# Optimization experiments

Measured on AMD Instinct MI355X. Metric: run time of the kernel, lower is better.

The kernel has to match this reference:

```python
import jax, jax.numpy as jnp
import numpy as np

N_NODES = 100000
N_EDGES = 1600000
IN_DIM = 128
OUT_DIM = 64


def setup_inputs() -> dict:
    key = jax.random.key(0)
    k1, k2, k3, k4, k5 = jax.random.split(key, 5)
    x = jax.random.normal(k1, (N_NODES, IN_DIM), dtype=jnp.float32)
    edge_index = jax.random.randint(k2, (2, N_EDGES), 0, N_NODES, dtype=jnp.int64)
    # xavier_uniform for Linear(in,out): bound = sqrt(6/(in+out))
    wb = float(np.sqrt(6.0 / (IN_DIM + OUT_DIM)))
    W = jax.random.uniform(k3, (OUT_DIM, IN_DIM), dtype=jnp.float32, minval=-wb, maxval=wb)
    # xavier_uniform on a.unsqueeze(0): fan_in=out_dim, fan_out=1
    ab = float(np.sqrt(6.0 / (OUT_DIM + 1)))
    a_src = jax.random.uniform(k4, (OUT_DIM,), dtype=jnp.float32, minval=-ab, maxval=b if (b := ab) else ab)
    a_dst = jax.random.uniform(k5, (OUT_DIM,), dtype=jnp.float32, minval=-ab, maxval=ab)
    return {"x": x, "edge_index": edge_index, "W": W, "a_src": a_src, "a_dst": a_dst}


def reference(x, edge_index, W, a_src, a_dst):
    # h = x @ W^T : [N, out_dim]
    h = x @ W.T
    src, dst = edge_index[0], edge_index[1]
    # per-node attention logits, gathered per edge (cheaper than gathering h twice for the dot)
    s_src = h @ a_src  # [N]
    s_dst = h @ a_dst  # [N]
    e = s_src[src] + s_dst[dst]  # [E]
    e = jnp.where(e >= 0, e, 0.2 * e)  # LeakyReLU(0.2)
    e = jnp.clip(e, -10.0, 10.0)
    alpha_num = jnp.exp(e)
    denom = jax.ops.segment_sum(alpha_num, dst, num_segments=N_NODES)  # [N]
    alpha = alpha_num / (denom[dst] + 1e-9)  # [E]; dropout is identity (eval / p=0)
    msgs = alpha[:, None] * h[src]  # [E, out_dim]
    out = jax.ops.segment_sum(msgs, dst, num_segments=N_NODES)  # [N, out_dim]
    return out
```

## Files before the change

### kernel.cpp

```cpp
#include <hip/hip_runtime.h>
#include <math.h>

#define NN 100000
#define NE 1600000
#define BKB 7
#define BSZ 128
#define NBKT 782
#define LPS  (NBKT + 1)
#define EPB 2048
#define NPB ((NE + EPB - 1) / EPB)
#define TOTC (NBKT * NPB)
#define SBLK 2048
#define NSB ((TOTC + SBLK - 1) / SBLK)
#define LBUF2 2560
#define EVC 5

typedef unsigned int uint;
typedef unsigned short ushort;
typedef __attribute__((ext_vector_type(8))) short bfx8;
typedef __attribute__((ext_vector_type(4))) float f32x4;

static __device__ __forceinline__ ushort f2bf(float f) {
  uint u = __float_as_uint(f);
  uint r = (u + 0x7fffu + ((u >> 16) & 1u)) >> 16;
  return (ushort)r;
}
static __device__ __forceinline__ float bf2f(ushort v) {
  return __uint_as_float((uint)v << 16);
}
static __device__ __forceinline__ bfx8 cvt8(float4 a, float4 b) {
  bfx8 r;
  r[0] = (short)f2bf(a.x); r[1] = (short)f2bf(a.y);
  r[2] = (short)f2bf(a.z); r[3] = (short)f2bf(a.w);
  r[4] = (short)f2bf(b.x); r[5] = (short)f2bf(b.y);
  r[6] = (short)f2bf(b.z); r[7] = (short)f2bf(b.w);
  return r;
}

__global__ __launch_bounds__(256) void k_h(
    const float* __restrict__ x, const float* __restrict__ W,
    const float* __restrict__ a_src, const float* __restrict__ a_dst,
    ushort* __restrict__ h16, float* __restrict__ ssrc, float* __restrict__ sdst)
{
  __shared__ __align__(16) ushort ws[64 * 128];
  const int t = threadIdx.x;
  const int base = blockIdx.x * 64;
  const float4* x4 = (const float4*)x;
  const float4* W4 = (const float4*)W;

#pragma unroll
  for (int q = 0; q < 8; ++q) {
    int f = q * 256 + t;
    int row = f >> 5, c4 = f & 31;
    float4 v = W4[f];
    ushort4 pk = make_ushort4(f2bf(v.x), f2bf(v.y), f2bf(v.z), f2bf(v.w));
    int byte = row * 256 + ((c4 * 8) ^ ((row & 7) << 4));
    *(ushort4*)((char*)ws + byte) = pk;
  }

  const int wid = t >> 6;
  const int lane = t & 63;
  const int lg = lane >> 4;
  const int lr = lane & 15;

  const int node = base + wid * 16 + lr;
  const bool ok = node < NN;
  const float4* xr = x4 + (size_t)node * 32;

  float4 xa[4][2];
#pragma unroll
  for (int ks = 0; ks < 4; ++ks) {
    xa[ks][0] = ok ? xr[ks * 8 + lg * 2]     : make_float4(0.f, 0.f, 0.f, 0.f);
    xa[ks][1] = ok ? xr[ks * 8 + lg * 2 + 1] : make_float4(0.f, 0.f, 0.f, 0.f);
  }
  __syncthreads();

  f32x4 acc[4];
#pragma unroll
  for (int ng = 0; ng < 4; ++ng) acc[ng] = (f32x4){0.f, 0.f, 0.f, 0.f};

#pragma unroll
  for (int ks = 0; ks < 4; ++ks) {
    int kb = ks * 64 + lg * 16;
    bfx8 af = cvt8(xa[ks][0], xa[ks][1]);
    bfx8 bfr[4];
#pragma unroll
    for (int ng = 0; ng < 4; ++ng) {
      int row = ng * 16 + lr;
      bfr[ng] = *(const bfx8*)((const char*)ws + row * 256 + (kb ^ ((row & 7) << 4)));
    }
#pragma unroll
    for (int ng = 0; ng < 4; ++ng)
      acc[ng] = __builtin_amdgcn_mfma_f32_16x16x32_bf16(af, bfr[ng], acc[ng], 0, 0, 0);
  }

  float as_[4], ad_[4];
#pragma unroll
  for (int ng = 0; ng < 4; ++ng) { as_[ng] = a_src[ng * 16 + lr]; ad_[ng] = a_dst[ng * 16 + lr]; }
#pragma unroll
  for (int r = 0; r < 4; ++r) {
    int nout = base + wid * 16 + lg * 4 + r;
    float ps = 0.f, pd = 0.f;
#pragma unroll
    for (int ng = 0; ng < 4; ++ng) { ps += acc[ng][r] * as_[ng]; pd += acc[ng][r] * ad_[ng]; }
#pragma unroll
    for (int m = 1; m < 16; m <<= 1) { ps += __shfl_xor(ps, m); pd += __shfl_xor(pd, m); }
    if (lr == 0 && nout < NN) { ssrc[nout] = ps; sdst[nout] = pd; }
    if (nout < NN) {
#pragma unroll
      for (int ng = 0; ng < 4; ++ng)
        h16[(size_t)nout * 64 + ng * 16 + lr] = f2bf(acc[ng][r]);
    }
  }
}

__global__ __launch_bounds__(512) void k_sort(const int* __restrict__ ei,
                                              int* __restrict__ cnt_cm,
                                              int* __restrict__ lpre,
                                              int* __restrict__ stage)
{
  __shared__ int hh[NBKT];
  __shared__ int sums[512];
  __shared__ int sbuf[EPB];
  const int t = threadIdx.x, c = blockIdx.x;
  for (int i = t; i < NBKT; i += 512) hh[i] = 0;
  __syncthreads();

  const int base = c * EPB;
  const int nloc = min(EPB, NE - base);
  int my_src[EPB / 512], my_dst[EPB / 512];
#pragma unroll
  for (int q = 0; q < EPB / 512; ++q) {
    int e = base + q * 512 + t;
    if (e < NE) {
      my_src[q] = ei[e];
      my_dst[q] = ei[NE + e];
      atomicAdd(&hh[my_dst[q] >> BKB], 1);
    } else my_dst[q] = -1;
  }
  __syncthreads();

  int i0 = 2 * t, i1 = 2 * t + 1;
  int v0 = (i0 < NBKT) ? hh[i0] : 0;
  int v1 = (i1 < NBKT) ? hh[i1] : 0;
  sums[t] = v0 + v1;
  __syncthreads();
  for (int off = 1; off < 512; off <<= 1) {
    int u = (t >= off) ? sums[t - off] : 0;
    __syncthreads();
    sums[t] += u;
    __syncthreads();
  }
  int ex0 = sums[t] - (v0 + v1);
  if (i0 < NBKT) {
    hh[i0] = ex0;
    lpre[c * LPS + i0] = ex0;
    cnt_cm[(size_t)c * NBKT + i0] = v0;
  }
  if (i1 < NBKT) {
    hh[i1] = ex0 + v0;
    lpre[c * LPS + i1] = ex0 + v0;
    cnt_cm[(size_t)c * NBKT + i1] = v1;
  }
  if (t == 0) lpre[c * LPS + NBKT] = nloc;
  __syncthreads();

#pragma unroll
  for (int q = 0; q < EPB / 512; ++q) {
    if (my_dst[q] >= 0) {
      int dst = my_dst[q], src = my_src[q];
      int pos = atomicAdd(&hh[dst >> BKB], 1);
      sbuf[pos] = src | ((dst & (BSZ - 1)) << 24);
    }
  }
  __syncthreads();
#pragma unroll
  for (int q = 0; q < EPB / 512; ++q) {
    int i = q * 512 + t;
    if (i < nloc) stage[base + i] = sbuf[i];
  }
}

__global__ __launch_bounds__(256) void k_tr(const int* __restrict__ cnt_cm,
                                            const int* __restrict__ lpre,
                                            int* __restrict__ cnt,
                                            int* __restrict__ lpreT)
{
  __shared__ int tileA[32][33];
  __shared__ int tileB[32][33];
  int cb = blockIdx.x * 32, bb = blockIdx.y * 32;
  int tx = threadIdx.x & 31, ty = threadIdx.x >> 5;
  for (int r = ty; r < 32; r += 8) {
    int c = cb + r, b = bb + tx;
    bool in = (c < NPB && b < NBKT);
    tileA[r][tx] = in ? cnt_cm[(size_t)c * NBKT + b] : 0;
    tileB[r][tx] = in ? lpre[(size_t)c * LPS + b] : 0;
  }
  __syncthreads();
  for (int r = ty; r < 32; r += 8) {
    int b = bb + r, c = cb + tx;
    if (b < NBKT && c < NPB) {
      cnt[(size_t)b * NPB + c] = tileA[tx][r];
      lpreT[(size_t)b * NPB + c] = tileB[tx][r];
    }
  }
}

__global__ __launch_bounds__(256) void k_scanA(const int* __restrict__ cnt,
                                               int* __restrict__ partials)
{
  __shared__ int sm[256];
  int t = threadIdx.x, b = blockIdx.x;
  const int4* c4 = (const int4*)(cnt + b * SBLK + t * 8);
  int4 u = c4[0], v = c4[1];
  sm[t] = u.x + u.y + u.z + u.w + v.x + v.y + v.z + v.w;
  __syncthreads();
  for (int s = 128; s > 0; s >>= 1) { if (t < s) sm[t] += sm[t + s]; __syncthreads(); }
  if (t == 0) partials[b] = sm[0];
}

__global__ __launch_bounds__(512) void k_scanB(int* __restrict__ partials,
                                               int* __restrict__ boff)
{
  __shared__ int sm[512];
  int t = threadIdx.x;
  int v = (t < NSB) ? partials[t] : 0;
  sm[t] = v;
  __syncthreads();
  for (int off = 1; off < 512; off <<= 1) {
    int u = (t >= off) ? sm[t - off] : 0;
    __syncthreads();
    sm[t] += u;
    __syncthreads();
  }
  if (t < NSB) partials[t] = sm[t] - v;
  if (t == 0) boff[NBKT] = NE;
}

__global__ __launch_bounds__(256) void k_scanC(int* __restrict__ cnt,
                                               const int* __restrict__ partials,
                                               int* __restrict__ boff)
{
  __shared__ int sm[256];
  int t = threadIdx.x, b = blockIdx.x;
  int base = b * SBLK + t * 8;
  int4* c4 = (int4*)(cnt + base);
  int4 u = c4[0], v = c4[1];
  int tot = u.x + u.y + u.z + u.w + v.x + v.y + v.z + v.w;
  sm[t] = tot;
  __syncthreads();
  for (int off = 1; off < 256; off <<= 1) {
    int w = (t >= off) ? sm[t - off] : 0;
    __syncthreads();
    sm[t] += w;
    __syncthreads();
  }
  int run = partials[b] + sm[t] - tot;
  int e[8] = {u.x, u.y, u.z, u.w, v.x, v.y, v.z, v.w};
  int ex[8];
#pragma unroll
  for (int k = 0; k < 8; ++k) { ex[k] = run; run += e[k]; }
#pragma unroll
  for (int k = 0; k < 8; ++k) {
    int idx = base + k;
    if (idx < TOTC && idx % NPB == 0) boff[idx / NPB] = ex[k];
  }
  c4[0] = make_int4(ex[0], ex[1], ex[2], ex[3]);
  c4[1] = make_int4(ex[4], ex[5], ex[6], ex[7]);
}

__global__ __launch_bounds__(512) void k_fuse(const int* __restrict__ boff,
                                              const int* __restrict__ pcnt,
                                              const int* __restrict__ lpreT,
                                              const int* __restrict__ stage,
                                              const float* __restrict__ ssrc,
                                              const float* __restrict__ sdst,
                                              const ushort* __restrict__ h16,
                                              float* __restrict__ out)
{
  __shared__ int2 lbuf[LBUF2];
  __shared__ int pcl[NPB + 1];
  __shared__ int lpb[NPB];
  __shared__ int nh[BSZ];
  __shared__ int nst[BSZ];
  __shared__ int cur[BSZ];
  __shared__ float sdl[BSZ];
  const int b = blockIdx.x, t = threadIdx.x;
  const int e_beg = boff[b], e_end = boff[b + 1];
  const int m = e_end - e_beg;

  for (int j = t; j < NPB; j += 512) {
    pcl[j] = pcnt[(size_t)b * NPB + j] - e_beg;
    lpb[j] = lpreT[(size_t)b * NPB + j];
  }
  if (t == 0) pcl[NPB] = m;
  if (t < BSZ) {
    nh[t] = 0;
    int node = (b << BKB) + t;
    sdl[t] = (node < NN) ? sdst[node] : 0.f;
  }
  __syncthreads();

  int ev[EVC];
  float ssv[EVC];
  int ne = 0;
#pragma unroll
  for (int q = 0; q < EVC; ++q) {
    int i = q * 512 + t;
    if (i < m) {
      int lo = 0, hi = NPB;
      while (hi - lo > 1) { int mid = (lo + hi) >> 1; if (pcl[mid] <= i) lo = mid; else hi = mid; }
      ev[q] = stage[(size_t)lo * EPB + lpb[lo] + (i - pcl[lo])];
      ssv[q] = ssrc[ev[q] & 0xFFFFFF];
      atomicAdd(&nh[((uint)ev[q]) >> 24], 1);
      ne = q + 1;
    }
  }
  __syncthreads();

  int v0 = (t < BSZ) ? nh[t] : 0;
  if (t < BSZ) nst[t] = v0;
  __syncthreads();
  for (int off = 1; off < BSZ; off <<= 1) {
    int u = (t >= off && t < BSZ) ? nst[t - off] : 0;
    __syncthreads();
    if (t < BSZ) nst[t] += u;
    __syncthreads();
  }
  if (t < BSZ) { int ex = nst[t] - v0; cur[t] = ex; nh[t] = ex; }
  __syncthreads();

  int slots[EVC];
  float alph[EVC];
#pragma unroll
  for (int q = 0; q < EVC; ++q) {
    if (q < ne) {
      int dl = ((uint)ev[q]) >> 24;
      slots[q] = atomicAdd(&cur[dl], 1);
      float e = ssv[q] + sdl[dl];
      e = (e >= 0.f) ? e : 0.2f * e;
      e = fminf(fmaxf(e, -10.f), 10.f);
      alph[q] = __expf(e);
    }
  }
#pragma unroll
  for (int q = 0; q < EVC; ++q)
    if (q < ne) lbuf[slots[q]] = make_int2(ev[q] & 0xFFFFFF, __float_as_int(alph[q]));
  __syncthreads();

  const int sid = t >> 4;
  const int l16 = t & 15;
  const int half = l16 >> 3, l8 = l16 & 7;
  const uint4* h4 = (const uint4*)h16;
#pragma unroll
  for (int r = 0; r < 4; ++r) {
    int nl = sid + 32 * r;
    int beg = nh[nl];
    int end = nst[nl];
    float a0 = 0.f, a1 = 0.f, a2 = 0.f, a3 = 0.f;
    float a4 = 0.f, a5 = 0.f, a6 = 0.f, a7 = 0.f;
    float den = 0.f;
    int last = end - 1;
    for (int j = beg; j < end; j += 8) {
#pragma unroll
      for (int p = 0; p < 4; ++p) {
        int idx = j + p * 2 + half;
        int2 e = lbuf[min(idx, last)];
        float a = (idx < end) ? __int_as_float(e.y) : 0.f;
        uint4 hq = h4[(size_t)e.x * 8 + l8];
        den += a;
        a0 += a * bf2f((ushort)(hq.x & 0xffff));
        a1 += a * bf2f((ushort)(hq.x >> 16));
        a2 += a * bf2f((ushort)(hq.y & 0xffff));
        a3 += a * bf2f((ushort)(hq.y >> 16));
        a4 += a * bf2f((ushort)(hq.z & 0xffff));
        a5 += a * bf2f((ushort)(hq.z >> 16));
        a6 += a * bf2f((ushort)(hq.w & 0xffff));
        a7 += a * bf2f((ushort)(hq.w >> 16));
      }
    }
    a0 += __shfl_xor(a0, 8);
    a1 += __shfl_xor(a1, 8);
    a2 += __shfl_xor(a2, 8);
    a3 += __shfl_xor(a3, 8);
    a4 += __shfl_xor(a4, 8);
    a5 += __shfl_xor(a5, 8);
    a6 += __shfl_xor(a6, 8);
    a7 += __shfl_xor(a7, 8);
    den += __shfl_xor(den, 8);
    int node = (b << BKB) + nl;
    if (node < NN) {
      float inv = 1.f / (den + 1e-9f);
      float4 o = half ? make_float4(a4 * inv, a5 * inv, a6 * inv, a7 * inv)
                      : make_float4(a0 * inv, a1 * inv, a2 * inv, a3 * inv);
      ((float4*)out)[(size_t)node * 16 + l8 * 2 + half] = o;
    }
  }
}

extern "C" void kernel_launch(void* const* d_in, const int* in_sizes, int n_in,
                              void* d_out, int out_size, void* d_ws, size_t ws_size,
                              hipStream_t stream)
{
  const float* x     = (const float*)d_in[0];
  const int*   ei    = (const int*)d_in[1];
  const float* W     = (const float*)d_in[2];
  const float* a_src = (const float*)d_in[3];
  const float* a_dst = (const float*)d_in[4];
  float* out = (float*)d_out;

  char* p = (char*)d_ws;
  auto alloc = [&](size_t bytes) -> char* {
    char* r = p;
    p += (bytes + 255) & ~(size_t)255;
    return r;
  };
  ushort* h16    = (ushort*)alloc((size_t)NN * 64 * 2);
  float* ssrc    = (float*)alloc((size_t)NN * 4);
  float* sdst    = (float*)alloc((size_t)NN * 4);
  int*   cnt     = (int*)alloc((size_t)NSB * SBLK * 4);
  int*   cnt_cm  = (int*)alloc((size_t)NPB * NBKT * 4);
  int*   lpre    = (int*)alloc((size_t)NPB * LPS * 4);
  int*   lpreT   = (int*)alloc((size_t)NBKT * NPB * 4);
  int*   boff    = (int*)alloc((size_t)(NBKT + 1) * 4);
  int*   partials= (int*)alloc((size_t)NSB * 4);
  int*   stage   = (int*)alloc((size_t)NPB * EPB * 4);

  k_h<<<(NN + 63) / 64, 256, 0, stream>>>(x, W, a_src, a_dst, h16, ssrc, sdst);
  k_sort<<<NPB, 512, 0, stream>>>(ei, cnt_cm, lpre, stage);
  k_tr<<<dim3((NPB + 31) / 32, (NBKT + 31) / 32), 256, 0, stream>>>(cnt_cm, lpre, cnt, lpreT);
  k_scanA<<<NSB, 256, 0, stream>>>(cnt, partials);
  k_scanB<<<1, 512, 0, stream>>>(partials, boff);
  k_scanC<<<NSB, 256, 0, stream>>>(cnt, partials, boff);
  k_fuse<<<NBKT, 512, 0, stream>>>(boff, cnt, lpreT, stage, ssrc, sdst, h16, out);
}
```

Baseline: 86.29 us.

## Merge projection and edge bucket-sort kernels into one interleaved launch

Combines the node projection GEMM kernel and the per-chunk edge bucket sort into a single launch. Even blocks compute 128 nodes of h, s_src and s_dst with 512 threads, and odd blocks perform the counting-sort of one edge chunk, sharing a 16KB shared-memory buffer. This removes one kernel launch boundary and lets the compute-bound MFMA work overlap with the memory- and atomic-bound sort work. The cost is a larger block size for the GEMM path and shared memory sized for the larger of the two roles, which may reduce occupancy. Block count HB+NPB (782+782) matches the even/odd interleave because HB equals NPB.

```diff
diff --git a/kernel.cpp b/kernel.cpp
--- a/kernel.cpp
+++ b/kernel.cpp
@@ -9,6 +9,7 @@
 #define LPS  (NBKT + 1)
 #define EPB 2048
 #define NPB ((NE + EPB - 1) / EPB)
+#define HB  782
 #define TOTC (NBKT * NPB)
 #define SBLK 2048
 #define NSB ((TOTC + SBLK - 1) / SBLK)
@@ -37,147 +38,149 @@
   return r;
 }
 
-__global__ __launch_bounds__(256) void k_h(
+__global__ __launch_bounds__(512) void k_hs(
     const float* __restrict__ x, const float* __restrict__ W,
     const float* __restrict__ a_src, const float* __restrict__ a_dst,
-    ushort* __restrict__ h16, float* __restrict__ ssrc, float* __restrict__ sdst)
-{
-  __shared__ __align__(16) ushort ws[64 * 128];
+    const int* __restrict__ ei,
+    ushort* __restrict__ h16, float* __restrict__ ssrc, float* __restrict__ sdst,
+    int* __restrict__ cnt_cm, int* __restrict__ lpre, int* __restrict__ stage)
+{
+  __shared__ __align__(16) char smem[16384];
   const int t = threadIdx.x;
-  const int base = blockIdx.x * 64;
-  const float4* x4 = (const float4*)x;
-  const float4* W4 = (const float4*)W;
-
-#pragma unroll
-  for (int q = 0; q < 8; ++q) {
-    int f = q * 256 + t;
-    int row = f >> 5, c4 = f & 31;
-    float4 v = W4[f];
-    ushort4 pk = make_ushort4(f2bf(v.x), f2bf(v.y), f2bf(v.z), f2bf(v.w));
-    int byte = row * 256 + ((c4 * 8) ^ ((row & 7) << 4));
-    *(ushort4*)((char*)ws + byte) = pk;
-  }
-
-  const int wid = t >> 6;
-  const int lane = t & 63;
-  const int lg = lane >> 4;
-  const int lr = lane & 15;
-
-  const int node = base + wid * 16 + lr;
-  const bool ok = node < NN;
-  const float4* xr = x4 + (size_t)node * 32;
-
-  float4 xa[4][2];
-#pragma unroll
-  for (int ks = 0; ks < 4; ++ks) {
-    xa[ks][0] = ok ? xr[ks * 8 + lg * 2]     : make_float4(0.f, 0.f, 0.f, 0.f);
-    xa[ks][1] = ok ? xr[ks * 8 + lg * 2 + 1] : make_float4(0.f, 0.f, 0.f, 0.f);
-  }
-  __syncthreads();
-
-  f32x4 acc[4];
-#pragma unroll
-  for (int ng = 0; ng < 4; ++ng) acc[ng] = (f32x4){0.f, 0.f, 0.f, 0.f};
-
-#pragma unroll
-  for (int ks = 0; ks < 4; ++ks) {
-    int kb = ks * 64 + lg * 16;
-    bfx8 af = cvt8(xa[ks][0], xa[ks][1]);
-    bfx8 bfr[4];
-#pragma unroll
-    for (int ng = 0; ng < 4; ++ng) {
-      int row = ng * 16 + lr;
-      bfr[ng] = *(const bfx8*)((const char*)ws + row * 256 + (kb ^ ((row & 7) << 4)));
-    }
-#pragma unroll
-    for (int ng = 0; ng < 4; ++ng)
-      acc[ng] = __builtin_amdgcn_mfma_f32_16x16x32_bf16(af, bfr[ng], acc[ng], 0, 0, 0);
-  }
-
-  float as_[4], ad_[4];
-#pragma unroll
-  for (int ng = 0; ng < 4; ++ng) { as_[ng] = a_src[ng * 16 + lr]; ad_[ng] = a_dst[ng * 16 + lr]; }
-#pragma unroll
-  for (int r = 0; r < 4; ++r) {
-    int nout = base + wid * 16 + lg * 4 + r;
-    float ps = 0.f, pd = 0.f;
-#pragma unroll
-    for (int ng = 0; ng < 4; ++ng) { ps += acc[ng][r] * as_[ng]; pd += acc[ng][r] * ad_[ng]; }
-#pragma unroll
-    for (int m = 1; m < 16; m <<= 1) { ps += __shfl_xor(ps, m); pd += __shfl_xor(pd, m); }
-    if (lr == 0 && nout < NN) { ssrc[nout] = ps; sdst[nout] = pd; }
-    if (nout < NN) {
+
+  if ((blockIdx.x & 1) == 0) {
+    ushort* ws = (ushort*)smem;
+    const int hb = blockIdx.x >> 1;
+    const int base = hb * 128;
+    const float4* x4 = (const float4*)x;
+    const float4* W4 = (const float4*)W;
+
+#pragma unroll
+    for (int q = 0; q < 4; ++q) {
+      int f = q * 512 + t;
+      int row = f >> 5, c4 = f & 31;
+      float4 v = W4[f];
+      ushort4 pk = make_ushort4(f2bf(v.x), f2bf(v.y), f2bf(v.z), f2bf(v.w));
+      int byte = row * 256 + ((c4 * 8) ^ ((row & 7) << 4));
+      *(ushort4*)((char*)ws + byte) = pk;
+    }
+
+    const int wid = t >> 6;
+    const int lane = t & 63;
+    const int lg = lane >> 4;
+    const int lr = lane & 15;
+
+    const int node = base + wid * 16 + lr;
+    const bool ok = node < NN;
+    const float4* xr = x4 + (size_t)node * 32;
+
+    float4 xa[4][2];
+#pragma unroll
+    for (int ks = 0; ks < 4; ++ks) {
+      xa[ks][0] = ok ? xr[ks * 8 + lg * 2]     : make_float4(0.f, 0.f, 0.f, 0.f);
+      xa[ks][1] = ok ? xr[ks * 8 + lg * 2 + 1] : make_float4(0.f, 0.f, 0.f, 0.f);
+    }
+    __syncthreads();
+
+    f32x4 acc[4];
+#pragma unroll
+    for (int ng = 0; ng < 4; ++ng) acc[ng] = (f32x4){0.f, 0.f, 0.f, 0.f};
+
+#pragma unroll
+    for (int ks = 0; ks < 4; ++ks) {
+      int kb = ks * 64 + lg * 16;
+      bfx8 af = cvt8(xa[ks][0], xa[ks][1]);
+      bfx8 bfr[4];
+#pragma unroll
+      for (int ng = 0; ng < 4; ++ng) {
+        int row = ng * 16 + lr;
+        bfr[ng] = *(const bfx8*)((const char*)ws + row * 256 + (kb ^ ((row & 7) << 4)));
+      }
 #pragma unroll
       for (int ng = 0; ng < 4; ++ng)
-        h16[(size_t)nout * 64 + ng * 16 + lr] = f2bf(acc[ng][r]);
-    }
-  }
-}
-
-__global__ __launch_bounds__(512) void k_sort(const int* __restrict__ ei,
-                                              int* __restrict__ cnt_cm,
-                                              int* __restrict__ lpre,
-                                              int* __restrict__ stage)
-{
-  __shared__ int hh[NBKT];
-  __shared__ int sums[512];
-  __shared__ int sbuf[EPB];
-  const int t = threadIdx.x, c = blockIdx.x;
-  for (int i = t; i < NBKT; i += 512) hh[i] = 0;
-  __syncthreads();
-
-  const int base = c * EPB;
-  const int nloc = min(EPB, NE - base);
-  int my_src[EPB / 512], my_dst[EPB / 512];
-#pragma unroll
-  for (int q = 0; q < EPB / 512; ++q) {
-    int e = base + q * 512 + t;
-    if (e < NE) {
-      my_src[q] = ei[e];
-      my_dst[q] = ei[NE + e];
-      atomicAdd(&hh[my_dst[q] >> BKB], 1);
-    } else my_dst[q] = -1;
-  }
-  __syncthreads();
-
-  int i0 = 2 * t, i1 = 2 * t + 1;
-  int v0 = (i0 < NBKT) ? hh[i0] : 0;
-  int v1 = (i1 < NBKT) ? hh[i1] : 0;
-  sums[t] = v0 + v1;
-  __syncthreads();
-  for (int off = 1; off < 512; off <<= 1) {
-    int u = (t >= off) ? sums[t - off] : 0;
-    __syncthreads();
-    sums[t] += u;
-    __syncthreads();
-  }
-  int ex0 = sums[t] - (v0 + v1);
-  if (i0 < NBKT) {
-    hh[i0] = ex0;
-    lpre[c * LPS + i0] = ex0;
-    cnt_cm[(size_t)c * NBKT + i0] = v0;
-  }
-  if (i1 < NBKT) {
-    hh[i1] = ex0 + v0;
-    lpre[c * LPS + i1] = ex0 + v0;
-    cnt_cm[(size_t)c * NBKT + i1] = v1;
-  }
-  if (t == 0) lpre[c * LPS + NBKT] = nloc;
-  __syncthreads();
-
-#pragma unroll
-  for (int q = 0; q < EPB / 512; ++q) {
-    if (my_dst[q] >= 0) {
-      int dst = my_dst[q], src = my_src[q];
-      int pos = atomicAdd(&hh[dst >> BKB], 1);
-      sbuf[pos] = src | ((dst & (BSZ - 1)) << 24);
-    }
-  }
-  __syncthreads();
-#pragma unroll
-  for (int q = 0; q < EPB / 512; ++q) {
-    int i = q * 512 + t;
-    if (i < nloc) stage[base + i] = sbuf[i];
+        acc[ng] = __builtin_amdgcn_mfma_f32_16x16x32_bf16(af, bfr[ng], acc[ng], 0, 0, 0);
+    }
+
+    float as_[4], ad_[4];
+#pragma unroll
+    for (int ng = 0; ng < 4; ++ng) { as_[ng] = a_src[ng * 16 + lr]; ad_[ng] = a_dst[ng * 16 + lr]; }
+#pragma unroll
+    for (int r = 0; r < 4; ++r) {
+      int nout = base + wid * 16 + lg * 4 + r;
+      float ps = 0.f, pd = 0.f;
+#pragma unroll
+      for (int ng = 0; ng < 4; ++ng) { ps += acc[ng][r] * as_[ng]; pd += acc[ng][r] * ad_[ng]; }
+#pragma unroll
+      for (int m = 1; m < 16; m <<= 1) { ps += __shfl_xor(ps, m); pd += __shfl_xor(pd, m); }
+      if (lr == 0 && nout < NN) { ssrc[nout] = ps; sdst[nout] = pd; }
+      if (nout < NN) {
+#pragma unroll
+        for (int ng = 0; ng < 4; ++ng)
+          h16[(size_t)nout * 64 + ng * 16 + lr] = f2bf(acc[ng][r]);
+      }
+    }
+  } else {
+    int* hh   = (int*)smem;
+    int* sums = (int*)(smem + 3200);
+    int* sbuf = (int*)(smem + 5248);
+    const int c = blockIdx.x >> 1;
+
+    for (int i = t; i < NBKT; i += 512) hh[i] = 0;
+    __syncthreads();
+
+    const int base = c * EPB;
+    const int nloc = min(EPB, NE - base);
+    int my_src[EPB / 512], my_dst[EPB / 512];
+#pragma unroll
+    for (int q = 0; q < EPB / 512; ++q) {
+      int e = base + q * 512 + t;
+      if (e < NE) {
+        my_src[q] = ei[e];
+        my_dst[q] = ei[NE + e];
+        atomicAdd(&hh[my_dst[q] >> BKB], 1);
+      } else my_dst[q] = -1;
+    }
+    __syncthreads();
+
+    int i0 = 2 * t, i1 = 2 * t + 1;
+    int v0 = (i0 < NBKT) ? hh[i0] : 0;
+    int v1 = (i1 < NBKT) ? hh[i1] : 0;
+    sums[t] = v0 + v1;
+    __syncthreads();
+    for (int off = 1; off < 512; off <<= 1) {
+      int u = (t >= off) ? sums[t - off] : 0;
+      __syncthreads();
+      sums[t] += u;
+      __syncthreads();
+    }
+    int ex0 = sums[t] - (v0 + v1);
+    if (i0 < NBKT) {
+      hh[i0] = ex0;
+      lpre[c * LPS + i0] = ex0;
+      cnt_cm[(size_t)c * NBKT + i0] = v0;
+    }
+    if (i1 < NBKT) {
+      hh[i1] = ex0 + v0;
+      lpre[c * LPS + i1] = ex0 + v0;
+      cnt_cm[(size_t)c * NBKT + i1] = v1;
+    }
+    if (t == 0) lpre[c * LPS + NBKT] = nloc;
+    __syncthreads();
+
+#pragma unroll
+    for (int q = 0; q < EPB / 512; ++q) {
+      if (my_dst[q] >= 0) {
+        int dst = my_dst[q], src = my_src[q];
+        int pos = atomicAdd(&hh[dst >> BKB], 1);
+        sbuf[pos] = src | ((dst & (BSZ - 1)) << 24);
+      }
+    }
+    __syncthreads();
+#pragma unroll
+    for (int q = 0; q < EPB / 512; ++q) {
+      int i = q * 512 + t;
+      if (i < nloc) stage[base + i] = sbuf[i];
+    }
   }
 }
 
@@ -426,8 +429,8 @@
   int*   partials= (int*)alloc((size_t)NSB * 4);
   int*   stage   = (int*)alloc((size_t)NPB * EPB * 4);
 
-  k_h<<<(NN + 63) / 64, 256, 0, stream>>>(x, W, a_src, a_dst, h16, ssrc, sdst);
-  k_sort<<<NPB, 512, 0, stream>>>(ei, cnt_cm, lpre, stage);
+  k_hs<<<HB + NPB, 512, 0, stream>>>(x, W, a_src, a_dst, ei,
+                                     h16, ssrc, sdst, cnt_cm, lpre, stage);
   k_tr<<<dim3((NPB + 31) / 32, (NBKT + 31) / 32), 256, 0, stream>>>(cnt_cm, lpre, cnt, lpreT);
   k_scanA<<<NSB, 256, 0, stream>>>(cnt, partials);
   k_scanB<<<1, 512, 0, stream>>>(partials, boff);
```

After: 87.03 us. No clear change (+0.9%).
